# Performance work log

Measured on AMD Instinct MI355X. Metric: run time of the kernel, lower is better.

Reference implementation:

```python
import jax, jax.numpy as jnp
import numpy as np

N = 4096
K = 8


def setup_inputs() -> dict:
    key = jax.random.key(0)
    kA, kb, ka, kZ, kC = jax.random.split(key, 5)
    A = (jax.random.uniform(kA, (N, N)) < 0.01).astype(jnp.float32)
    beta = jax.random.normal(kb, (N,), dtype=jnp.float32)
    a = jax.random.normal(ka, (1,), dtype=jnp.float32)
    Z = jax.random.normal(kZ, (K, N), dtype=jnp.float32)
    C = jax.random.normal(kC, (N, K), dtype=jnp.float32)
    return {"A": A, "beta": beta, "a": a, "Z": Z, "C": C}


def reference(A, beta, a, Z, C):
    # beta_ij = beta_i + beta_j  -> [N, N]
    beta2 = beta[:, None] + beta[None, :]
    Zs = jax.nn.softmax(Z, axis=0)          # [K, N], softmax over archetypes
    Cs = jax.nn.softmax(C, axis=0)          # [N, K], softmax over nodes
    # M = (Zs @ Cs @ Zs).T -> [N, K] latent positions
    M = (Zs @ (Cs @ Zs)).T
    # Pairwise euclidean distance with the original's +1e-6 shift inside the square.
    diff = M[:, None, :] - M[None, :, :] + 1e-6   # [N, N, K]
    z_dist = jnp.sqrt(jnp.sum(diff * diff, axis=-1))  # [N, N]
    theta = beta2 - a[0] * z_dist
    sp = jax.nn.softplus(theta)
    # Zero the diagonal (theta - diag(diagonal(theta)) zeroes diag entries).
    d = jnp.arange(N)
    theta_off = theta.at[d, d].set(0.0)
    sp_off = sp.at[d, d].set(0.0)
    LL = jnp.sum(theta_off * A) - jnp.sum(sp_off)
    return LL
```

## Files before the change

kernel.cpp:

```cpp
#include <hip/hip_runtime.h>

#define N 4096
#define K 8
#define RB 64
#define CB 256
#define RCH 8
#define NCH (RB / RCH)
#define NPB 16

__device__ __forceinline__ float fast_exp2(float x) { return __builtin_amdgcn_exp2f(x); }
__device__ __forceinline__ float fast_log2(float x) { return __builtin_amdgcn_logf(x); }
__device__ __forceinline__ float fast_sqrt(float x) { return __builtin_amdgcn_sqrtf(x); }

__device__ __forceinline__ void load_lds_16B(const float* g, float* l) {
    __builtin_amdgcn_global_load_lds((const __attribute__((address_space(1))) void*)g,
                                     (__attribute__((address_space(3))) void*)l,
                                     16, 0, 0);
}

__global__ __launch_bounds__(256) void prep_stats(
    const float* __restrict__ Z, const float* __restrict__ C,
    const float* __restrict__ A, const float* __restrict__ beta,
    const float* __restrict__ a_ptr,
    float* __restrict__ ZsT, float* __restrict__ Upart, float* __restrict__ out)
{
    const int t = threadIdx.x;
    const int n = blockIdx.x * 256 + t;
    const float L2E = 1.44269504f;
    const float LN2 = 0.69314718f;

    __shared__ float zsL[256 * K];
    __shared__ float eL[256 * K];
    __shared__ float red[4][64];
    __shared__ float dsum[4];

    const float av_diag = A[(size_t)n * N + n];
    const float bn = beta[n];
    const float a_v = a_ptr[0];

    float z[K];
#pragma unroll
    for (int k = 0; k < K; ++k) z[k] = Z[k * N + n];
    float zmax = z[0];
#pragma unroll
    for (int k = 1; k < K; ++k) zmax = fmaxf(zmax, z[k]);
    float zs[K];
    float zsum = 0.f;
#pragma unroll
    for (int k = 0; k < K; ++k) { zs[k] = fast_exp2((z[k] - zmax) * L2E); zsum += zs[k]; }
    const float inv = 1.f / zsum;
#pragma unroll
    for (int k = 0; k < K; ++k) zs[k] *= inv;

    float4* zst_p = (float4*)(ZsT + (size_t)n * K);
    zst_p[0] = make_float4(zs[0], zs[1], zs[2], zs[3]);
    zst_p[1] = make_float4(zs[4], zs[5], zs[6], zs[7]);

    const float4* c_p = (const float4*)(C + (size_t)n * K);
    const float4 c0 = c_p[0], c1 = c_p[1];
    float e[K];
    e[0] = fast_exp2(c0.x * L2E); e[1] = fast_exp2(c0.y * L2E);
    e[2] = fast_exp2(c0.z * L2E); e[3] = fast_exp2(c0.w * L2E);
    e[4] = fast_exp2(c1.x * L2E); e[5] = fast_exp2(c1.y * L2E);
    e[6] = fast_exp2(c1.z * L2E); e[7] = fast_exp2(c1.w * L2E);

#pragma unroll
    for (int k = 0; k < K; ++k) { zsL[t * K + k] = zs[k]; eL[t * K + k] = e[k]; }
    __syncthreads();

    const int cell = t & 63, q = t >> 6;
    const int a = cell >> 3, b = cell & 7;
    float s = 0.f;
    const int n0 = q * 64;
#pragma unroll 4
    for (int nn = 0; nn < 64; ++nn)
        s = fmaf(zsL[(n0 + nn) * K + a], eL[(n0 + nn) * K + b], s);
    red[q][cell] = s;
    __syncthreads();
    if (t < 64)
        Upart[blockIdx.x * 64 + t] = red[0][t] + red[1][t] + red[2][t] + red[3][t];

    const float theta = fmaf(-a_v, 2.8284271247e-6f, 2.f * bn);
    const float ex = fast_exp2(theta * L2E);
    const float sp = LN2 * fast_log2(1.f + ex);
    float d = fmaf(theta, av_diag, -sp);
    for (int off = 32; off > 0; off >>= 1) d += __shfl_down(d, off, 64);
    const int lane = t & 63, wd = t >> 6;
    if (lane == 0) dsum[wd] = d;
    __syncthreads();
    if (t == 0) atomicAdd(out, -(dsum[0] + dsum[1] + dsum[2] + dsum[3]));
}

__global__ __launch_bounds__(256) void pair_ll(
    const float* __restrict__ A, const float* __restrict__ beta,
    const float* __restrict__ a_ptr, const float* __restrict__ ZsT,
    const float* __restrict__ Upart, float* __restrict__ out)
{
    const int t = threadIdx.x;
    const int lane = t & 63, w = t >> 6;
    const int i0 = blockIdx.x * RB;
    const int jbase = blockIdx.y * CB;
    const int j = jbase + t;
    const float L2E = 1.44269504f;
    const float LN2 = 0.69314718f;

    __shared__ __align__(16) float Abuf[2][RCH][CB];
    __shared__ __align__(16) float4 ntwoMi[RB][2];
    __shared__ __align__(8)  float2 rc[RB];
    __shared__ float UL[64];
    __shared__ float wsum[4];

    {
        const float* g = A + (size_t)(i0 + w * 2) * N + jbase + lane * 4;
        load_lds_16B(g,     &Abuf[0][w * 2][0]);
        load_lds_16B(g + N, &Abuf[0][w * 2 + 1][0]);
    }

    if (t < 64) {
        float s = 0.f;
#pragma unroll
        for (int blk = 0; blk < NPB; ++blk) s += Upart[blk * 64 + t];
        UL[t] = s;
    }
    __syncthreads();

    float sinv[8];
#pragma unroll
    for (int b = 0; b < 8; ++b) {
        float s = 0.f;
#pragma unroll
        for (int a = 0; a < 8; ++a) s += UL[a * 8 + b];
        sinv[b] = 1.f / s;
    }

    const float4* zp = (const float4*)(ZsT + (size_t)j * K);
    const float4 z0 = zp[0], z1 = zp[1];
    float wv[K] = { z0.x * sinv[0], z0.y * sinv[1], z0.z * sinv[2], z0.w * sinv[3],
                    z1.x * sinv[4], z1.y * sinv[5], z1.z * sinv[6], z1.w * sinv[7] };
    float mj[K];
#pragma unroll
    for (int k = 0; k < K; ++k) {
        float acc = 0.f;
#pragma unroll
        for (int kk = 0; kk < K; ++kk) acc = fmaf(UL[k * K + kk], wv[kk], acc);
        mj[k] = acc;
    }
    float mj2 = mj[0] * mj[0];
#pragma unroll
    for (int k = 1; k < K; ++k) mj2 = fmaf(mj[k], mj[k], mj2);
    const float bjL2E = beta[j] * L2E;
    const float naL2E = -a_ptr[0] * L2E;

    if (t < RB) {
        const float4* zp2 = (const float4*)(ZsT + (size_t)(i0 + t) * K);
        const float4 y0 = zp2[0], y1 = zp2[1];
        float wr[K] = { y0.x * sinv[0], y0.y * sinv[1], y0.z * sinv[2], y0.w * sinv[3],
                        y1.x * sinv[4], y1.y * sinv[5], y1.z * sinv[6], y1.w * sinv[7] };
        float v[K];
#pragma unroll
        for (int k = 0; k < K; ++k) {
            float acc = 0.f;
#pragma unroll
            for (int kk = 0; kk < K; ++kk) acc = fmaf(UL[k * K + kk], wr[kk], acc);
            v[k] = acc + 1e-6f;
        }
        float s2 = 0.f;
#pragma unroll
        for (int k = 0; k < K; ++k) s2 = fmaf(v[k], v[k], s2);
        ntwoMi[t][0] = make_float4(-2.f * v[0], -2.f * v[1], -2.f * v[2], -2.f * v[3]);
        ntwoMi[t][1] = make_float4(-2.f * v[4], -2.f * v[5], -2.f * v[6], -2.f * v[7]);
        rc[t] = make_float2(s2, beta[i0 + t] * L2E);
    }
    __syncthreads();

    float acc_t = 0.f, acc_l = 0.f;
    int buf = 0;
    for (int c = 0; c < NCH; ++c) {
        if (c + 1 < NCH) {
            const float* g = A + (size_t)(i0 + (c + 1) * RCH + w * 2) * N + jbase + lane * 4;
            load_lds_16B(g,     &Abuf[buf ^ 1][w * 2][0]);
            load_lds_16B(g + N, &Abuf[buf ^ 1][w * 2 + 1][0]);
        }
#pragma unroll
        for (int r = 0; r < RCH; ++r) {
            const int ir = c * RCH + r;
            const float av = Abuf[buf][r][t];
            const float4 tm0 = ntwoMi[ir][0];
            const float4 tm1 = ntwoMi[ir][1];
            const float2 cc = rc[ir];
            float ss = cc.x + mj2;
            ss = fmaf(tm0.x, mj[0], ss); ss = fmaf(tm0.y, mj[1], ss);
            ss = fmaf(tm0.z, mj[2], ss); ss = fmaf(tm0.w, mj[3], ss);
            ss = fmaf(tm1.x, mj[4], ss); ss = fmaf(tm1.y, mj[5], ss);
            ss = fmaf(tm1.z, mj[6], ss); ss = fmaf(tm1.w, mj[7], ss);
            ss = fmaxf(ss, 0.f);
            const float dist = fast_sqrt(ss);
            const float t2 = fmaf(naL2E, dist, cc.y + bjL2E);
            const float ex = fast_exp2(t2);
            const float lp = fast_log2(1.f + ex);
            acc_t = fmaf(t2, av, acc_t);
            acc_l += lp;
        }
        if (c + 1 < NCH) __syncthreads();
        buf ^= 1;
    }
    float acc = LN2 * (acc_t - acc_l);

    for (int off = 32; off > 0; off >>= 1) acc += __shfl_down(acc, off, 64);
    if (lane == 0) wsum[w] = acc;
    __syncthreads();
    if (t == 0) atomicAdd(out, wsum[0] + wsum[1] + wsum[2] + wsum[3]);
}

extern "C" void kernel_launch(void* const* d_in, const int* in_sizes, int n_in,
                              void* d_out, int out_size, void* d_ws, size_t ws_size,
                              hipStream_t stream)
{
    const float* A    = (const float*)d_in[0];
    const float* beta = (const float*)d_in[1];
    const float* a    = (const float*)d_in[2];
    const float* Z    = (const float*)d_in[3];
    const float* C    = (const float*)d_in[4];
    float* out = (float*)d_out;

    float* ws    = (float*)d_ws;
    float* ZsT   = ws;
    float* Upart = ws + (size_t)N * K;

    hipMemsetAsync(out, 0, sizeof(float), stream);

    prep_stats<<<NPB, 256, 0, stream>>>(Z, C, A, beta, a, ZsT, Upart, out);

    dim3 grid(N / RB, N / CB);
    pair_ll<<<grid, 256, 0, stream>>>(A, beta, a, ZsT, Upart, out);
}
```

Baseline: 112.8 us.

## Replace LDS double-buffered A staging with register double-buffered direct loads

Drops the global_load_lds double buffer and its per-chunk __syncthreads. Each thread now loads its own column of A straight into two register banks of 8 values, prefetching the next 8 rows while computing on the current ones. It also adds an occupancy hint of 6 blocks per CU to launch_bounds. The cost being targeted is the block barrier and LDS traffic; in exchange each load is a 4-byte scalar instead of a 16-byte one, and register pressure goes up.

```diff
diff --git a/kernel.cpp b/kernel.cpp
--- a/kernel.cpp
+++ b/kernel.cpp
@@ -4,19 +4,11 @@
 #define K 8
 #define RB 64
 #define CB 256
-#define RCH 8
-#define NCH (RB / RCH)
 #define NPB 16
 
 __device__ __forceinline__ float fast_exp2(float x) { return __builtin_amdgcn_exp2f(x); }
 __device__ __forceinline__ float fast_log2(float x) { return __builtin_amdgcn_logf(x); }
 __device__ __forceinline__ float fast_sqrt(float x) { return __builtin_amdgcn_sqrtf(x); }
-
-__device__ __forceinline__ void load_lds_16B(const float* g, float* l) {
-    __builtin_amdgcn_global_load_lds((const __attribute__((address_space(1))) void*)g,
-                                     (__attribute__((address_space(3))) void*)l,
-                                     16, 0, 0);
-}
 
 __global__ __launch_bounds__(256) void prep_stats(
     const float* __restrict__ Z, const float* __restrict__ C,
@@ -91,7 +83,7 @@
     if (t == 0) atomicAdd(out, -(dsum[0] + dsum[1] + dsum[2] + dsum[3]));
 }
 
-__global__ __launch_bounds__(256) void pair_ll(
+__global__ __launch_bounds__(256, 6) void pair_ll(
     const float* __restrict__ A, const float* __restrict__ beta,
     const float* __restrict__ a_ptr, const float* __restrict__ ZsT,
     const float* __restrict__ Upart, float* __restrict__ out)
@@ -104,17 +96,41 @@
     const float L2E = 1.44269504f;
     const float LN2 = 0.69314718f;
 
-    __shared__ __align__(16) float Abuf[2][RCH][CB];
     __shared__ __align__(16) float4 ntwoMi[RB][2];
     __shared__ __align__(8)  float2 rc[RB];
     __shared__ float UL[64];
     __shared__ float wsum[4];
 
-    {
-        const float* g = A + (size_t)(i0 + w * 2) * N + jbase + lane * 4;
-        load_lds_16B(g,     &Abuf[0][w * 2][0]);
-        load_lds_16B(g + N, &Abuf[0][w * 2 + 1][0]);
-    }
+    const float* ga = A + (size_t)i0 * N + j;
+
+    float avA[8], avB[8];
+
+#define LOADB(BANK, BB)                                                        \
+    _Pragma("unroll")                                                          \
+    for (int r = 0; r < 8; ++r) BANK[r] = ga[(size_t)((BB) * 8 + r) * N];
+
+#define COMP(BANK, BB)                                                         \
+    _Pragma("unroll")                                                          \
+    for (int r = 0; r < 8; ++r) {                                              \
+        const int ir = (BB) * 8 + r;                                           \
+        const float4 tm0 = ntwoMi[ir][0];                  \
+        const float4 tm1 = ntwoMi[ir][1];                                      \
+        const float2 cc = rc[ir];                                              \
+        float ss = cc.x + mj2;                                                 \
+        ss = fmaf(tm0.x, mj[0], ss); ss = fmaf(tm0.y, mj[1], ss);              \
+        ss = fmaf(tm0.z, mj[2], ss); ss = fmaf(tm0.w, mj[3], ss);              \
+        ss = fmaf(tm1.x, mj[4], ss); ss = fmaf(tm1.y, mj[5], ss);              \
+        ss = fmaf(tm1.z, mj[6], ss); ss = fmaf(tm1.w, mj[7], ss);              \
+        ss = fmaxf(ss, 0.f);                           \
+        const float dist = fast_sqrt(ss);                                      \
+        const float t2 = fmaf(naL2E, dist, cc.y + bjL2E);                      \
+        const float ex = fast_exp2(t2);                                        \
+        const float lp = fast_log2(1.f + ex);                                  \
+        acc_t = fmaf(t2, BANK[r], acc_t);                                      \
+        acc_l += lp;                                                           \
+    }
+
+    LOADB(avA, 0)
 
     if (t < 64) {
         float s = 0.f;
@@ -174,36 +190,16 @@
     __syncthreads();
 
     float acc_t = 0.f, acc_l = 0.f;
-    int buf = 0;
-    for (int c = 0; c < NCH; ++c) {
-        if (c + 1 < NCH) {
-            const float* g = A + (size_t)(i0 + (c + 1) * RCH + w * 2) * N + jbase + lane * 4;
-            load_lds_16B(g,     &Abuf[buf ^ 1][w * 2][0]);
-            load_lds_16B(g + N, &Abuf[buf ^ 1][w * 2 + 1][0]);
-        }
-#pragma unroll
-        for (int r = 0; r < RCH; ++r) {
-            const int ir = c * RCH + r;
-            const float av = Abuf[buf][r][t];
-            const float4 tm0 = ntwoMi[ir][0];
-            const float4 tm1 = ntwoMi[ir][1];
-            const float2 cc = rc[ir];
-            float ss = cc.x + mj2;
-            ss = fmaf(tm0.x, mj[0], ss); ss = fmaf(tm0.y, mj[1], ss);
-            ss = fmaf(tm0.z, mj[2], ss); ss = fmaf(tm0.w, mj[3], ss);
-            ss = fmaf(tm1.x, mj[4], ss); ss = fmaf(tm1.y, mj[5], ss);
-            ss = fmaf(tm1.z, mj[6], ss); ss = fmaf(tm1.w, mj[7], ss);
-            ss = fmaxf(ss, 0.f);
-            const float dist = fast_sqrt(ss);
-            const float t2 = fmaf(naL2E, dist, cc.y + bjL2E);
-            const float ex = fast_exp2(t2);
-            const float lp = fast_log2(1.f + ex);
-            acc_t = fmaf(t2, av, acc_t);
-            acc_l += lp;
-        }
-        if (c + 1 < NCH) __syncthreads();
-        buf ^= 1;
-    }
+
+    LOADB(avB, 1)  COMP(avA, 0)
+    LOADB(avA, 2)  COMP(avB, 1)
+    LOADB(avB, 3)  COMP(avA, 2)
+    LOADB(avA, 4)  COMP(avB, 3)
+    LOADB(avB, 5)  COMP(avA, 4)
+    LOADB(avA, 6)  COMP(avB, 5)
+    LOADB(avB, 7)  COMP(avA, 6)
+                   COMP(avB, 7)
+
     float acc = LN2 * (acc_t - acc_l);
 
     for (int off = 32; off > 0; off >>= 1) acc += __shfl_down(acc, off, 64);
```

Result: slower. 131.8 us (+16.8%).
